# Performance work log

Measured on AMD Instinct MI355X. Metric: run time of the kernel, lower is better.

The kernel has to match this reference:

```python
import jax, jax.numpy as jnp
import numpy as np

B, T, C, H = 512, 256, 384, 64  # batch, seq (block_size), n_embd, head_size
SCALE = C ** 0.5  # NOTE: source multiplies by C**0.5 (faithful to original)


def setup_inputs() -> dict:
    key = jax.random.key(0)
    kx, kq, kk, kv = jax.random.split(key, 4)
    lim = 1.0 / np.sqrt(C)
    return {
        "x": jax.random.normal(kx, (B, T, C), dtype=jnp.float32),
        "Wq": jax.random.uniform(kq, (C, H), jnp.float32, -lim, lim),
        "Wk": jax.random.uniform(kk, (C, H), jnp.float32, -lim, lim),
        "Wv": jax.random.uniform(kv, (C, H), jnp.float32, -lim, lim),
    }


def reference(x, Wq, Wk, Wv):
    q = jnp.einsum("btc,ch->bth", x, Wq)
    k = jnp.einsum("btc,ch->bth", x, Wk)
    v = jnp.einsum("btc,ch->bth", x, Wv)
    wei = jnp.einsum("bth,bsh->bts", q, k) * SCALE  # [B,T,T]
    causal = jnp.tril(jnp.ones((T, T), dtype=bool))
    wei = jnp.where(causal, wei, -jnp.inf)
    wei = jax.nn.softmax(wei, axis=-1)
    # dropout is identity in eval mode
    out = jnp.einsum("bts,bsh->bth", wei, v)
    return out
```

## Files before the change

### kernel.cpp

```cpp
#include <hip/hip_runtime.h>
#include <math.h>

#define B_ 512
#define T_ 256
#define C_ 384
#define H_ 64

typedef __attribute__((ext_vector_type(8))) short bf16x8;
typedef __attribute__((ext_vector_type(4))) float f32x4;

#define MFMA16(a, b, c) __builtin_amdgcn_mfma_f32_16x16x32_bf16((a), (b), (c), 0, 0, 0)

#define SM_KHI   0u
#define SM_KLO   36864u
#define SM_VT    73728u
#define SM_WQH   73728u
#define SM_WQL   78848u
#define SM_WKH   83968u
#define SM_WKL   89088u
#define SM_WVH   94208u
#define SM_WVL   99328u
#define SM_XREG  107520u
#define SM_XH    107520u
#define SM_XL    128000u
#define SM_QS(s) (SM_XREG + (unsigned)(s)*9216u)
#define SM_PS(w) (SM_XREG + (unsigned)(w)*2304u)
#define SM_BYTES 148480u

static __device__ __forceinline__ unsigned short bhi(float x) {
    return (unsigned short)(__float_as_uint(x) >> 16);
}
static __device__ __forceinline__ unsigned short blo(float x) {
    float h = __uint_as_float((__float_as_uint(x) >> 16) << 16);
    return (unsigned short)(__float_as_uint(x - h) >> 16);
}
static __device__ __forceinline__ unsigned short brne(float x) {
    unsigned u = __float_as_uint(x);
    return (unsigned short)((u + 0x7FFFu + ((u >> 16) & 1u)) >> 16);
}
static __device__ __forceinline__ unsigned pk_hi(float a, float b) {
    return (unsigned)bhi(a) | ((unsigned)bhi(b) << 16);
}
static __device__ __forceinline__ unsigned pk_lo(float a, float b) {
    return (unsigned)blo(a) | ((unsigned)blo(b) << 16);
}

__global__ __launch_bounds__(512, 2)
void head_mfma(const float* __restrict__ x,
               const float* __restrict__ Wq,
               const float* __restrict__ Wk,
               const float* __restrict__ Wv,
               float* __restrict__ out)
{
    __shared__ __align__(16) unsigned char sm[SM_BYTES];

    const int tid  = threadIdx.x;
    const int b    = blockIdx.x;
    const int w    = tid >> 6;
    const int lane = tid & 63;
    const int l15  = lane & 15;
    const int quad = lane >> 4;
    const int rA   = w * 16;
    const int rB   = 240 - w * 16;

    f32x4 qac[2][4], kac[2][4], vac[2][4];
    #pragma unroll
    for (int mt = 0; mt < 2; ++mt)
        #pragma unroll
        for (int nt = 0; nt < 4; ++nt) {
            f32x4 z = {0.f, 0.f, 0.f, 0.f};
            qac[mt][nt] = z; kac[mt][nt] = z; vac[mt][nt] = z;
        }

    const int xrowi = tid >> 1;
    const int xhalf = tid & 1;
    const float* xrow = x + ((size_t)b * T_ + xrowi) * C_ + xhalf * 16;
    const int hW = tid >> 3;
    const int cg = tid & 7;

    float4 xb[4];
    float  wbq[4], wbk[4], wbv[4];
    {
        const float4* xp = (const float4*)(xrow);
        #pragma unroll
        for (int j = 0; j < 4; ++j) xb[j] = xp[j];
        const float* q0 = Wq + (size_t)(cg * 4) * H_ + hW;
        const float* k0 = Wk + (size_t)(cg * 4) * H_ + hW;
        const float* v0 = Wv + (size_t)(cg * 4) * H_ + hW;
        #pragma unroll
        for (int j = 0; j < 4; ++j) { wbq[j] = q0[j*H_]; wbk[j] = k0[j*H_]; wbv[j] = v0[j*H_]; }
    }

    #pragma unroll 1
    for (int cc = 0; cc < 12; ++cc) {
        #pragma unroll
        for (int j = 0; j < 4; ++j) {
            uint2 hh, ll;
            hh.x = pk_hi(xb[j].x, xb[j].y); hh.y = pk_hi(xb[j].z, xb[j].w);
            ll.x = pk_lo(xb[j].x, xb[j].y); ll.y = pk_lo(xb[j].z, xb[j].w);
            *(uint2*)&sm[SM_XH + (unsigned)(xrowi*80 + xhalf*32 + j*8)] = hh;
            *(uint2*)&sm[SM_XL + (unsigned)(xrowi*80 + xhalf*32 + j*8)] = ll;
        }
        {
            const unsigned wo = (unsigned)(hW*80 + cg*8);
            uint2 t;
            t.x = pk_hi(wbq[0],wbq[1]); t.y = pk_hi(wbq[2],wbq[3]); *(uint2*)&sm[SM_WQH + wo] = t;
            t.x = pk_lo(wbq[0],wbq[1]); t.y = pk_lo(wbq[2],wbq[3]); *(uint2*)&sm[SM_WQL + wo] = t;
            t.x = pk_hi(wbk[0],wbk[1]); t.y = pk_hi(wbk[2],wbk[3]); *(uint2*)&sm[SM_WKH + wo] = t;
            t.x = pk_lo(wbk[0],wbk[1]); t.y = pk_lo(wbk[2],wbk[3]); *(uint2*)&sm[SM_WKL + wo] = t;
            t.x = pk_hi(wbv[0],wbv[1]); t.y = pk_hi(wbv[2],wbv[3]); *(uint2*)&sm[SM_WVH + wo] = t;
            t.x = pk_lo(wbv[0],wbv[1]); t.y = pk_lo(wbv[2],wbv[3]); *(uint2*)&sm[SM_WVL + wo] = t;
        }
        __syncthreads();

        if (cc < 11) {
            const float4* xp = (const float4*)(xrow + (cc + 1) * 32);
            #pragma unroll
            for (int j = 0; j < 4; ++j) xb[j] = xp[j];
            const size_t c0 = (size_t)((cc + 1) * 32 + cg * 4) * H_ + hW;
            #pragma unroll
            for (int j = 0; j < 4; ++j) {
                wbq[j] = Wq[c0 + (size_t)j*H_];
                wbk[j] = Wk[c0 + (size_t)j*H_];
                wbv[j] = Wv[c0 + (size_t)j*H_];
            }
        }

        bf16x8 ah[2], al[2];
        {
            const unsigned roA = (unsigned)((rA + l15)*80 + quad*16);
            const unsigned roB = (unsigned)((rB + l15)*80 + quad*16);
            ah[0] = *(const bf16x8*)&sm[SM_XH + roA];
            al[0] = *(const bf16x8*)&sm[SM_XL + roA];
            ah[1] = *(const bf16x8*)&sm[SM_XH + roB];
            al[1] = *(const bf16x8*)&sm[SM_XL + roB];
        }
#define PROJ_MAT(WTH, WTL, ACC)                                               \
        {                                                                     \
            bf16x8 bh[4], bl[4];                                              \
            _Pragma("unroll")                                                 \
            for (int nt = 0; nt < 4; ++nt) {                                  \
                const unsigned bo = (unsigned)((nt*16 + l15)*80 + quad*16);   \
                bh[nt] = *(const bf16x8*)&sm[(WTH) + bo];                     \
                bl[nt] = *(const bf16x8*)&sm[(WTL) + bo];                     \
            }                                                                 \
            _Pragma("unroll")                                                 \
            for (int mt = 0; mt < 2; ++mt)                                    \
                _Pragma("unroll")                                             \
                for (int nt = 0; nt < 4; ++nt) {                              \
                    f32x4 a = ACC[mt][nt];                                    \
                    a = MFMA16(al[mt], bh[nt], a);                            \
                    a = MFMA16(ah[mt], bl[nt], a);                            \
                    a = MFMA16(ah[mt], bh[nt], a);                            \
                    ACC[mt][nt] = a;                                          \
                }                                                             \
        }
        PROJ_MAT(SM_WQH, SM_WQL, qac)
        PROJ_MAT(SM_WKH, SM_WKL, kac)
        PROJ_MAT(SM_WVH, SM_WVL, vac)
        __syncthreads();
    }

    constexpr float SCALE = 19.595917942265423f;
    #pragma unroll
    for (int mt = 0; mt < 2; ++mt) {
        const int r0m = mt ? rB : rA;
        #pragma unroll
        for (int nt = 0; nt < 4; ++nt) {
            const f32x4 kv = kac[mt][nt];
            const f32x4 vv = vac[mt][nt];
            #pragma unroll
            for (int r = 0; r < 4; ++r) {
                const int row = r0m + quad*4 + r;
                const int h   = nt*16 + l15;
                *(unsigned short*)&sm[SM_KHI + (unsigned)(row*144 + h*2)] = bhi(kv[r]);
                *(unsigned short*)&sm[SM_KLO + (unsigned)(row*144 + h*2)] = blo(kv[r]);
                *(unsigned short*)&sm[SM_VT  + (unsigned)(h*528 + row*2)] = brne(vv[r]);
            }
        }
    }

    bf16x8 qAh[2][2], qAl[2][2];
    const int slot = w & 3;
#define Q_XPOSE()                                                             \
    {                                                                         \
        const unsigned qb = SM_QS(slot);                                      \
        _Pragma("unroll")                                                     \
        for (int mt = 0; mt < 2; ++mt)                                        \
            _Pragma("unroll")                                                 \
            for (int nt = 0; nt < 4; ++nt) {                                  \
                const f32x4 qv = qac[mt][nt];                                 \
                _Pragma("unroll")                                             \
                for (int r = 0; r < 4; ++r) {                                 \
                    const float qs = qv[r] * SCALE;                           \
                    const int rl = mt*16 + quad*4 + r;                        \
                    const int h  = nt*16 + l15;                               \
                    *(unsigned short*)&sm[qb +         (unsigned)(rl*144 + h*2)] = bhi(qs); \
                    *(unsigned short*)&sm[qb + 4608u + (unsigned)(rl*144 + h*2)] = blo(qs); \
                }                                                             \
            }                                                                 \
        _Pragma("unroll")                                                     \
        for (int mt = 0; mt < 2; ++mt)                                        \
            _Pragma("unroll")                                                 \
            for (int ks = 0; ks < 2; ++ks) {                                  \
                const unsigned qo = (unsigned)((mt*16 + l15)*144 + ks*64 + quad*16); \
                qAh[mt][ks] = *(const bf16x8*)&sm[qb + qo];                   \
                qAl[mt][ks] = *(const bf16x8*)&sm[qb + 4608u + qo];           \
            }                                                                 \
    }
    if (w < 4) Q_XPOSE();
    __syncthreads();
    if (w >= 4) Q_XPOSE();
    __syncthreads();

    f32x4 oac[2][4];
    float m_[2][4], l_[2][4];
    #pragma unroll
    for (int mt = 0; mt < 2; ++mt) {
        #pragma unroll
        for (int nt = 0; nt < 4; ++nt) { f32x4 z = {0.f,0.f,0.f,0.f}; oac[mt][nt] = z; }
        #pragma unroll
        for (int r = 0; r < 4; ++r) { m_[mt][r] = -1e30f; l_[mt][r] = 0.f; }
    }
    const unsigned pb = SM_PS(w);

    #pragma unroll
    for (int tile = 0; tile < 2; ++tile) {
        const int r0    = tile ? rB : rA;
        const int kbmax = tile ? ((15 - w) >> 2) : (w >> 2);
        #pragma unroll 1
        for (int kb = 0; kb <= kbmax; ++kb) {
            bf16x8 kbh[4][2], kbl[4][2];
            #pragma unroll
            for (int nt = 0; nt < 4; ++nt)
                #pragma unroll
                for (int ks = 0; ks < 2; ++ks) {
                    const unsigned ko = (unsigned)((kb*64 + nt*16 + l15)*144 + ks*64 + quad*16);
                    kbh[nt][ks] = *(const bf16x8*)&sm[SM_KHI + ko];
                    kbl[nt][ks] = *(const bf16x8*)&sm[SM_KLO + ko];
                }
            f32x4 sac[4];
            #pragma unroll
            for (int nt = 0; nt < 4; ++nt) {
                f32x4 a = {0.f,0.f,0.f,0.f};
                #pragma unroll
                for (int ks = 0; ks < 2; ++ks) {
                    a = MFMA16(qAl[tile][ks], kbh[nt][ks], a);
                    a = MFMA16(qAh[tile][ks], kbl[nt][ks], a);
                    a = MFMA16(qAh[tile][ks], kbh[nt][ks], a);
                }
                sac[nt] = a;
            }
            if (kb == kbmax) {
                #pragma unroll
                for (int nt = 0; nt < 4; ++nt)
                    #pragma unroll
                    for (int r = 0; r < 4; ++r) {
                        const int rg = r0 + quad*4 + r;
                        const int kl = kb*64 + nt*16 + l15;
                        if (kl > rg) sac[nt][r] = -1e30f;
                    }
            }
            #pragma unroll
            for (int r = 0; r < 4; ++r) {
                float v = fmaxf(fmaxf(sac[0][r], sac[1][r]), fmaxf(sac[2][r], sac[3][r]));
                v = fmaxf(v, __shfl_xor(v, 1)); v = fmaxf(v, __shfl_xor(v, 2));
                v = fmaxf(v, __shfl_xor(v, 4)); v = fmaxf(v, __shfl_xor(v, 8));
                const float mnew  = fmaxf(m_[tile][r], v);
                const float alpha = __expf(m_[tile][r] - mnew);
                m_[tile][r] = mnew;
                float rs = 0.f;
                #pragma unroll
                for (int nt = 0; nt < 4; ++nt) {
                    const float p = __expf(sac[nt][r] - mnew);
                    sac[nt][r] = p;
                    rs += p;
                }
                rs += __shfl_xor(rs, 1); rs += __shfl_xor(rs, 2);
                rs += __shfl_xor(rs, 4); rs += __shfl_xor(rs, 8);
                l_[tile][r] = l_[tile][r] * alpha + rs;
                #pragma unroll
                for (int nt = 0; nt < 4; ++nt) oac[tile][nt][r] *= alpha;
                const int rl = quad*4 + r;
                #pragma unroll
                for (int nt = 0; nt < 4; ++nt)
                    *(unsigned short*)&sm[pb + (unsigned)(rl*144 + (nt*16 + l15)*2)] =
                        brne(sac[nt][r]);
            }
            bf16x8 pA[2], vB[4][2];
            #pragma unroll
            for (int ks = 0; ks < 2; ++ks)
                pA[ks] = *(const bf16x8*)&sm[pb + (unsigned)(l15*144 + ks*64 + quad*16)];
            #pragma unroll
            for (int nt = 0; nt < 4; ++nt)
                #pragma unroll
                for (int ks = 0; ks < 2; ++ks)
                    vB[nt][ks] = *(const bf16x8*)&sm[SM_VT + (unsigned)((nt*16 + l15)*528 + kb*128 + ks*64 + quad*16)];
            #pragma unroll
            for (int nt = 0; nt < 4; ++nt) {
                f32x4 a = oac[tile][nt];
                a = MFMA16(pA[0], vB[nt][0], a);
                a = MFMA16(pA[1], vB[nt][1], a);
                oac[tile][nt] = a;
            }
        }
    }

    float* ob = out + (size_t)b * (T_ * H_);
    #pragma unroll
    for (int mt = 0; mt < 2; ++mt) {
        const int r0m = mt ? rB : rA;
        float inv[4];
        #pragma unroll
        for (int r = 0; r < 4; ++r) inv[r] = 1.0f / l_[mt][r];
        #pragma unroll
        for (int nt = 0; nt < 4; ++nt)
            #pragma unroll
            for (int r = 0; r < 4; ++r) {
                const int row = r0m + quad*4 + r;
                const int h   = nt*16 + l15;
                ob[row*64 + h] = oac[mt][nt][r] * inv[r];
            }
    }
}

extern "C" void kernel_launch(void* const* d_in, const int* in_sizes, int n_in,
                              void* d_out, int out_size, void* d_ws, size_t ws_size,
                              hipStream_t stream)
{
    const float* x  = (const float*)d_in[0];
    const float* Wq = (const float*)d_in[1];
    const float* Wk = (const float*)d_in[2];
    const float* Wv = (const float*)d_in[3];
    head_mfma<<<dim3(B_), dim3(512), 0, stream>>>(x, Wq, Wk, Wv, (float*)d_out);
}
```

Measured before the change: 330.0 us.

## Double block to 1024 threads with one 16-row tile per wave

The block grows from 512 to 1024 threads, so each of 16 waves now owns a single 16-row query tile. Previously each of 8 waves handled a balanced pair of tiles (rows w*16 and 240-w*16). Projection staging, Q transpose slots and attention loops are re-indexed for the finer split, which halves accumulators per wave and doubles the waves available to hide latency. In exchange, causal work is now uneven across waves (1 to 4 key blocks each), and the 1024-thread launch bound caps registers per wave.

```diff
diff --git a/kernel.cpp b/kernel.cpp
--- a/kernel.cpp
+++ b/kernel.cpp
@@ -23,7 +23,7 @@
 #define SM_XREG  107520u
 #define SM_XH    107520u
 #define SM_XL    128000u
-#define SM_QS(s) (SM_XREG + (unsigned)(s)*9216u)
+#define SM_QS(s) (SM_XREG + (unsigned)(s)*4608u)
 #define SM_PS(w) (SM_XREG + (unsigned)(w)*2304u)
 #define SM_BYTES 148480u
 
@@ -45,7 +45,7 @@
     return (unsigned)blo(a) | ((unsigned)blo(b) << 16);
 }
 
-__global__ __launch_bounds__(512, 2)
+__global__ __launch_bounds__(1024, 4)
 void head_mfma(const float* __restrict__ x,
                const float* __restrict__ Wq,
                const float* __restrict__ Wk,
@@ -61,79 +61,70 @@
     const int l15  = lane & 15;
     const int quad = lane >> 4;
     const int rA   = w * 16;
-    const int rB   = 240 - w * 16;
-
-    f32x4 qac[2][4], kac[2][4], vac[2][4];
-    #pragma unroll
-    for (int mt = 0; mt < 2; ++mt)
-        #pragma unroll
-        for (int nt = 0; nt < 4; ++nt) {
-            f32x4 z = {0.f, 0.f, 0.f, 0.f};
-            qac[mt][nt] = z; kac[mt][nt] = z; vac[mt][nt] = z;
-        }
-
-    const int xrowi = tid >> 1;
-    const int xhalf = tid & 1;
-    const float* xrow = x + ((size_t)b * T_ + xrowi) * C_ + xhalf * 16;
-    const int hW = tid >> 3;
-    const int cg = tid & 7;
-
-    float4 xb[4];
-    float  wbq[4], wbk[4], wbv[4];
+
+    f32x4 qac[4], kac[4], vac[4];
+    #pragma unroll
+    for (int nt = 0; nt < 4; ++nt) {
+        f32x4 z = {0.f, 0.f, 0.f, 0.f};
+        qac[nt] = z; kac[nt] = z; vac[nt] = z;
+    }
+
+    const int xrowi = tid >> 2;
+    const int xq    = tid & 3;
+    const float* xrow = x + ((size_t)b * T_ + xrowi) * C_ + xq * 8;
+    const int hW = tid >> 4;
+    const int cg = tid & 15;
+
+    float4 xb[2];
+    float  wbq[2], wbk[2], wbv[2];
     {
         const float4* xp = (const float4*)(xrow);
-        #pragma unroll
-        for (int j = 0; j < 4; ++j) xb[j] = xp[j];
-        const float* q0 = Wq + (size_t)(cg * 4) * H_ + hW;
-        const float* k0 = Wk + (size_t)(cg * 4) * H_ + hW;
-        const float* v0 = Wv + (size_t)(cg * 4) * H_ + hW;
-        #pragma unroll
-        for (int j = 0; j < 4; ++j) { wbq[j] = q0[j*H_]; wbk[j] = k0[j*H_]; wbv[j] = v0[j*H_]; }
+        xb[0] = xp[0]; xb[1] = xp[1];
+        const float* q0 = Wq + (size_t)(cg * 2) * H_ + hW;
+        const float* k0 = Wk + (size_t)(cg * 2) * H_ + hW;
+        const float* v0 = Wv + (size_t)(cg * 2) * H_ + hW;
+        #pragma unroll
+        for (int j = 0; j < 2; ++j) { wbq[j] = q0[j*H_]; wbk[j] = k0[j*H_]; wbv[j] = v0[j*H_]; }
     }
 
     #pragma unroll 1
     for (int cc = 0; cc < 12; ++cc) {
         #pragma unroll
-        for (int j = 0; j < 4; ++j) {
+        for (int j = 0; j < 2; ++j) {
             uint2 hh, ll;
             hh.x = pk_hi(xb[j].x, xb[j].y); hh.y = pk_hi(xb[j].z, xb[j].w);
             ll.x = pk_lo(xb[j].x, xb[j].y); ll.y = pk_lo(xb[j].z, xb[j].w);
-            *(uint2*)&sm[SM_XH + (unsigned)(xrowi*80 + xhalf*32 + j*8)] = hh;
-            *(uint2*)&sm[SM_XL + (unsigned)(xrowi*80 + xhalf*32 + j*8)] = ll;
+            *(uint2*)&sm[SM_XH + (unsigned)(xrowi*80 + xq*16 + j*8)] = hh;
+            *(uint2*)&sm[SM_XL + (unsigned)(xrowi*80 + xq*16 + j*8)] = ll;
         }
         {
-            const unsigned wo = (unsigned)(hW*80 + cg*8);
-            uint2 t;
-            t.x = pk_hi(wbq[0],wbq[1]); t.y = pk_hi(wbq[2],wbq[3]); *(uint2*)&sm[SM_WQH + wo] = t;
-            t.x = pk_lo(wbq[0],wbq[1]); t.y = pk_lo(wbq[2],wbq[3]); *(uint2*)&sm[SM_WQL + wo] = t;
-            t.x = pk_hi(wbk[0],wbk[1]); t.y = pk_hi(wbk[2],wbk[3]); *(uint2*)&sm[SM_WKH + wo] = t;
-            t.x = pk_lo(wbk[0],wbk[1]); t.y = pk_lo(wbk[2],wbk[3]); *(uint2*)&sm[SM_WKL + wo] = t;
-            t.x = pk_hi(wbv[0],wbv[1]); t.y = pk_hi(wbv[2],wbv[3]); *(uint2*)&sm[SM_WVH + wo] = t;
-            t.x = pk_lo(wbv[0],wbv[1]); t.y = pk_lo(wbv[2],wbv[3]); *(uint2*)&sm[SM_WVL + wo] = t;
+            const unsigned wo = (unsigned)(hW*80 + cg*4);
+            *(unsigned*)&sm[SM_WQH + wo] = pk_hi(wbq[0], wbq[1]);
+            *(unsigned*)&sm[SM_WQL + wo] = pk_lo(wbq[0], wbq[1]);
+            *(unsigned*)&sm[SM_WKH + wo] = pk_hi(wbk[0], wbk[1]);
+            *(unsigned*)&sm[SM_WKL + wo] = pk_lo(wbk[0], wbk[1]);
+            *(unsigned*)&sm[SM_WVH + wo] = pk_hi(wbv[0], wbv[1]);
+            *(unsigned*)&sm[SM_WVL + wo] = pk_lo(wbv[0], wbv[1]);
         }
         __syncthreads();
 
         if (cc < 11) {
             const float4* xp = (const float4*)(xrow + (cc + 1) * 32);
-            #pragma unroll
-            for (int j = 0; j < 4; ++j) xb[j] = xp[j];
-            const size_t c0 = (size_t)((cc + 1) * 32 + cg * 4) * H_ + hW;
-            #pragma unroll
-            for (int j = 0; j < 4; ++j) {
+            xb[0] = xp[0]; xb[1] = xp[1];
+            const size_t c0 = (size_t)((cc + 1) * 32 + cg * 2) * H_ + hW;
+            #pragma unroll
+            for (int j = 0; j < 2; ++j) {
                 wbq[j] = Wq[c0 + (size_t)j*H_];
                 wbk[j] = Wk[c0 + (size_t)j*H_];
                 wbv[j] = Wv[c0 + (size_t)j*H_];
             }
         }
 
-        bf16x8 ah[2], al[2];
+        bf16x8 ah, al;
         {
-            const unsigned roA = (unsigned)((rA + l15)*80 + quad*16);
-            const unsigned roB = (unsigned)((rB + l15)*80 + quad*16);
-            ah[0] = *(const bf16x8*)&sm[SM_XH + roA];
-            al[0] = *(const bf16x8*)&sm[SM_XL + roA];
-            ah[1] = *(const bf16x8*)&sm[SM_XH + roB];
-            al[1] = *(const bf16x8*)&sm[SM_XL + roB];
+            const unsigned ro = (unsigned)((rA + l15)*80 + quad*16);
+            ah = *(const bf16x8*)&sm[SM_XH + ro];
+            al = *(const bf16x8*)&sm[SM_XL + ro];
         }
 #define PROJ_MAT(WTH, WTL, ACC)                                               \
         {                                                                     \
@@ -145,15 +136,13 @@
                 bl[nt] = *(const bf16x8*)&sm[(WTL) + bo];                     \
             }                                                                 \
             _Pragma("unroll")                                                 \
-            for (int mt = 0; mt < 2; ++mt)                                    \
-                _Pragma("unroll")                                             \
-                for (int nt = 0; nt < 4; ++nt) {                              \
-                    f32x4 a = ACC[mt][nt];                                    \
-                    a = MFMA16(al[mt], bh[nt], a);                            \
-                    a = MFMA16(ah[mt], bl[nt], a);                            \
-                    a = MFMA16(ah[mt], bh[nt], a);                            \
-                    ACC[mt][nt] = a;                                          \
-                }                                                             \
+            for (int nt = 0; nt < 4; ++nt) {                                  \
+                f32x4 a = ACC[nt];                                            \
+                a = MFMA16(al, bh[nt], a);                                    \
+                a = MFMA16(ah, bl[nt], a);                                    \
+                a = MFMA16(ah, bh[nt], a);                                    \
+                ACC[nt] = a;                                                  \
+            }                                                                 \
         }
         PROJ_MAT(SM_WQH, SM_WQL, qac)
         PROJ_MAT(SM_WKH, SM_WKL, kac)
@@ -163,165 +152,146 @@
 
     constexpr float SCALE = 19.595917942265423f;
     #pragma unroll
-    for (int mt = 0; mt < 2; ++mt) {
-        const int r0m = mt ? rB : rA;
-        #pragma unroll
-        for (int nt = 0; nt < 4; ++nt) {
-            const f32x4 kv = kac[mt][nt];
-            const f32x4 vv = vac[mt][nt];
-            #pragma unroll
-            for (int r = 0; r < 4; ++r) {
-                const int row = r0m + quad*4 + r;
-                const int h   = nt*16 + l15;
-                *(unsigned short*)&sm[SM_KHI + (unsigned)(row*144 + h*2)] = bhi(kv[r]);
-                *(unsigned short*)&sm[SM_KLO + (unsigned)(row*144 + h*2)] = blo(kv[r]);
-                *(unsigned short*)&sm[SM_VT  + (unsigned)(h*528 + row*2)] = brne(vv[r]);
-            }
-        }
-    }
-
-    bf16x8 qAh[2][2], qAl[2][2];
-    const int slot = w & 3;
+    for (int nt = 0; nt < 4; ++nt) {
+        const f32x4 kv = kac[nt];
+        const f32x4 vv = vac[nt];
+        #pragma unroll
+        for (int r = 0; r < 4; ++r) {
+            const int row = rA + quad*4 + r;
+            const int h   = nt*16 + l15;
+            *(unsigned short*)&sm[SM_KHI + (unsigned)(row*144 + h*2)] = bhi(kv[r]);
+            *(unsigned short*)&sm[SM_KLO + (unsigned)(row*144 + h*2)] = blo(kv[r]);
+            *(unsigned short*)&sm[SM_VT  + (unsigned)(h*528 + row*2)] = brne(vv[r]);
+        }
+    }
+
+    bf16x8 qAh[2], qAl[2];
+    const int slot = w & 7;
 #define Q_XPOSE()                                                             \
     {                                                                         \
         const unsigned qb = SM_QS(slot);                                      \
         _Pragma("unroll")                                                     \
-        for (int mt = 0; mt < 2; ++mt)                                        \
+        for (int nt = 0; nt < 4; ++nt) {                                      \
+            const f32x4 qv = qac[nt];                                         \
             _Pragma("unroll")                                                 \
-            for (int nt = 0; nt < 4; ++nt) {                                  \
-                const f32x4 qv = qac[mt][nt];                                 \
-                _Pragma("unroll")                                             \
-                for (int r = 0; r < 4; ++r) {                                 \
-                    const float qs = qv[r] * SCALE;                           \
-                    const int rl = mt*16 + quad*4 + r;                        \
-                    const int h  = nt*16 + l15;                               \
-                    *(unsigned short*)&sm[qb +         (unsigned)(rl*144 + h*2)] = bhi(qs); \
-                    *(unsigned short*)&sm[qb + 4608u + (unsigned)(rl*144 + h*2)] = blo(qs); \
-                }                                                             \
+            for (int r = 0; r < 4; ++r) {                                     \
+                const float qs = qv[r] * SCALE;                               \
+                const int rl = quad*4 + r;                                    \
+                const int h  = nt*16 + l15;                                   \
+                *(unsigned short*)&sm[qb +         (unsigned)(rl*144 + h*2)] = bhi(qs); \
+                *(unsigned short*)&sm[qb + 2304u + (unsigned)(rl*144 + h*2)] = blo(qs); \
             }                                                                 \
+        }                                                                     \
         _Pragma("unroll")                                                     \
-        for (int mt = 0; mt < 2; ++mt)                                        \
-            _Pragma("unroll")                                                 \
-            for (int ks = 0; ks < 2; ++ks) {                                  \
-                const unsigned qo = (unsigned)((mt*16 + l15)*144 + ks*64 + quad*16); \
-                qAh[mt][ks] = *(const bf16x8*)&sm[qb + qo];                   \
-                qAl[mt][ks] = *(const bf16x8*)&sm[qb + 4608u + qo];           \
-            }                                                                 \
-    }
-    if (w < 4) Q_XPOSE();
+        for (int ks = 0; ks < 2; ++ks) {                                      \
+            const unsigned qo = (unsigned)(l15*144 + ks*64 + quad*16);        \
+            qAh[ks] = *(const bf16x8*)&sm[qb + qo];                           \
+            qAl[ks] = *(const bf16x8*)&sm[qb + 2304u + qo];                   \
+        }                                                                     \
+    }
+    if (w < 8) Q_XPOSE();
     __syncthreads();
-    if (w >= 4) Q_XPOSE();
+    if (w >= 8) Q_XPOSE();
     __syncthreads();
 
-    f32x4 oac[2][4];
-    float m_[2][4], l_[2][4];
-    #pragma unroll
-    for (int mt = 0; mt < 2; ++mt) {
-        #pragma unroll
-        for (int nt = 0; nt < 4; ++nt) { f32x4 z = {0.f,0.f,0.f,0.f}; oac[mt][nt] = z; }
-        #pragma unroll
-        for (int r = 0; r < 4; ++r) { m_[mt][r] = -1e30f; l_[mt][r] = 0.f; }
-    }
+    f32x4 oac[4];
+    float m_[4], l_[4];
+    #pragma unroll
+    for (int nt = 0; nt < 4; ++nt) { f32x4 z = {0.f,0.f,0.f,0.f}; oac[nt] = z; }
+    #pragma unroll
+    for (int r = 0; r < 4; ++r) { m_[r] = -1e30f; l_[r] = 0.f; }
     const unsigned pb = SM_PS(w);
-
-    #pragma unroll
-    for (int tile = 0; tile < 2; ++tile) {
-        const int r0    = tile ? rB : rA;
-        const int kbmax = tile ? ((15 - w) >> 2) : (w >> 2);
-        #pragma unroll 1
-        for (int kb = 0; kb <= kbmax; ++kb) {
-            bf16x8 kbh[4][2], kbl[4][2];
+    const int kbmax = w >> 2;
+
+    #pragma unroll 1
+    for (int kb = 0; kb <= kbmax; ++kb) {
+        bf16x8 kbh[4][2], kbl[4][2];
+        #pragma unroll
+        for (int nt = 0; nt < 4; ++nt)
+            #pragma unroll
+            for (int ks = 0; ks < 2; ++ks) {
+                const unsigned ko = (unsigned)((kb*64 + nt*16 + l15)*144 + ks*64 + quad*16);
+                kbh[nt][ks] = *(const bf16x8*)&sm[SM_KHI + ko];
+                kbl[nt][ks] = *(const bf16x8*)&sm[SM_KLO + ko];
+            }
+        f32x4 sac[4];
+        #pragma unroll
+        for (int nt = 0; nt < 4; ++nt) {
+            f32x4 a = {0.f,0.f,0.f,0.f};
+            #pragma unroll
+            for (int ks = 0; ks < 2; ++ks) {
+                a = MFMA16(qAl[ks], kbh[nt][ks], a);
+                a = MFMA16(qAh[ks], kbl[nt][ks], a);
+                a = MFMA16(qAh[ks], kbh[nt][ks], a);
+            }
+            sac[nt] = a;
+        }
+        if (kb == kbmax) {
             #pragma unroll
             for (int nt = 0; nt < 4; ++nt)
                 #pragma unroll
-                for (int ks = 0; ks < 2; ++ks) {
-                    const unsigned ko = (unsigned)((kb*64 + nt*16 + l15)*144 + ks*64 + quad*16);
-                    kbh[nt][ks] = *(const bf16x8*)&sm[SM_KHI + ko];
-                    kbl[nt][ks] = *(const bf16x8*)&sm[SM_KLO + ko];
+                for (int r = 0; r < 4; ++r) {
+                    const int rg = rA + quad*4 + r;
+                    const int kl = kb*64 + nt*16 + l15;
+                    if (kl > rg) sac[nt][r] = -1e30f;
                 }
-            f32x4 sac[4];
+        }
+        #pragma unroll
+        for (int r = 0; r < 4; ++r) {
+            float v = fmaxf(fmaxf(sac[0][r], sac[1][r]), fmaxf(sac[2][r], sac[3][r]));
+            v = fmaxf(v, __shfl_xor(v, 1)); v = fmaxf(v, __shfl_xor(v, 2));
+            v = fmaxf(v, __shfl_xor(v, 4)); v = fmaxf(v, __shfl_xor(v, 8));
+            const float mnew  = fmaxf(m_[r], v);
+            const float alpha = __expf(m_[r] - mnew);
+            m_[r] = mnew;
+            float rs = 0.f;
             #pragma unroll
             for (int nt = 0; nt < 4; ++nt) {
-                f32x4 a = {0.f,0.f,0.f,0.f};
-                #pragma unroll
-                for (int ks = 0; ks < 2; ++ks) {
-                    a = MFMA16(qAl[tile][ks], kbh[nt][ks], a);
-                    a = MFMA16(qAh[tile][ks], kbl[nt][ks], a);
-                    a = MFMA16(qAh[tile][ks], kbh[nt][ks], a);
-                }
-                sac[nt] = a;
+                const float p = __expf(sac[nt][r] - mnew);
+                sac[nt][r] = p;
+                rs += p;
             }
-            if (kb == kbmax) {
-                #pragma unroll
-                for (int nt = 0; nt < 4; ++nt)
-                    #pragma unroll
-                    for (int r = 0; r < 4; ++r) {
-                        const int rg = r0 + quad*4 + r;
-                        const int kl = kb*64 + nt*16 + l15;
-                        if (kl > rg) sac[nt][r] = -1e30f;
-                    }
-            }
-            #pragma unroll
-            for (int r = 0; r < 4; ++r) {
-                float v = fmaxf(fmaxf(sac[0][r], sac[1][r]), fmaxf(sac[2][r], sac[3][r]));
-                v = fmaxf(v, __shfl_xor(v, 1)); v = fmaxf(v, __shfl_xor(v, 2));
-                v = fmaxf(v, __shfl_xor(v, 4)); v = fmaxf(v, __shfl_xor(v, 8));
-                const float mnew  = fmaxf(m_[tile][r], v);
-                const float alpha = __expf(m_[tile][r] - mnew);
-                m_[tile][r] = mnew;
-                float rs = 0.f;
-                #pragma unroll
-                for (int nt = 0; nt < 4; ++nt) {
-                    const float p = __expf(sac[nt][r] - mnew);
-                    sac[nt][r] = p;
-                    rs += p;
-                }
-                rs += __shfl_xor(rs, 1); rs += __shfl_xor(rs, 2);
-                rs += __shfl_xor(rs, 4); rs += __shfl_xor(rs, 8);
-                l_[tile][r] = l_[tile][r] * alpha + rs;
-                #pragma unroll
-                for (int nt = 0; nt < 4; ++nt) oac[tile][nt][r] *= alpha;
-                const int rl = quad*4 + r;
-                #pragma unroll
-                for (int nt = 0; nt < 4; ++nt)
-                    *(unsigned short*)&sm[pb + (unsigned)(rl*144 + (nt*16 + l15)*2)] =
-                        brne(sac[nt][r]);
-            }
-            bf16x8 pA[2], vB[4][2];
+            rs += __shfl_xor(rs, 1); rs += __shfl_xor(rs, 2);
+            rs += __shfl_xor(rs, 4); rs += __shfl_xor(rs, 8);
+            l_[r] = l_[r] * alpha + rs;
+            #pragma unroll
+            for (int nt = 0; nt < 4; ++nt) oac[nt][r] *= alpha;
+            const int rl = quad*4 + r;
+            #pragma unroll
+            for (int nt = 0; nt < 4; ++nt)
+                *(unsigned short*)&sm[pb + (unsigned)(rl*144 + (nt*16 + l15)*2)] =
+                    brne(sac[nt][r]);
+        }
+        bf16x8 pA[2], vB[4][2];
+        #pragma unroll
+        for (int ks = 0; ks < 2; ++ks)
+            pA[ks] = *(const bf16x8*)&sm[pb + (unsigned)(l15*144 + ks*64 + quad*16)];
+        #pragma unroll
+        for (int nt = 0; nt < 4; ++nt)
             #pragma unroll
             for (int ks = 0; ks < 2; ++ks)
-                pA[ks] = *(const bf16x8*)&sm[pb + (unsigned)(l15*144 + ks*64 + quad*16)];
-            #pragma unroll
-            for (int nt = 0; nt < 4; ++nt)
-                #pragma unroll
-                for (int ks = 0; ks < 2; ++ks)
-                    vB[nt][ks] = *(const bf16x8*)&sm[SM_VT + (unsigned)((nt*16 + l15)*528 + kb*128 + ks*64 + quad*16)];
-            #pragma unroll
-            for (int nt = 0; nt < 4; ++nt) {
-                f32x4 a = oac[tile][nt];
-                a = MFMA16(pA[0], vB[nt][0], a);
-                a = MFMA16(pA[1], vB[nt][1], a);
-                oac[tile][nt] = a;
-            }
+                vB[nt][ks] = *(const bf16x8*)&sm[SM_VT + (unsigned)((nt*16 + l15)*528 + kb*128 + ks*64 + quad*16)];
+        #pragma unroll
+        for (int nt = 0; nt < 4; ++nt) {
+            f32x4 a = oac[nt];
+            a = MFMA16(pA[0], vB[nt][0], a);
+            a = MFMA16(pA[1], vB[nt][1], a);
+            oac[nt] = a;
         }
     }
 
     float* ob = out + (size_t)b * (T_ * H_);
-    #pragma unroll
-    for (int mt = 0; mt < 2; ++mt) {
-        const int r0m = mt ? rB : rA;
-        float inv[4];
-        #pragma unroll
-        for (int r = 0; r < 4; ++r) inv[r] = 1.0f / l_[mt][r];
-        #pragma unroll
-        for (int nt = 0; nt < 4; ++nt)
-            #pragma unroll
-            for (int r = 0; r < 4; ++r) {
-                const int row = r0m + quad*4 + r;
-                const int h   = nt*16 + l15;
-                ob[row*64 + h] = oac[mt][nt][r] * inv[r];
-            }
-    }
+    float inv[4];
+    #pragma unroll
+    for (int r = 0; r < 4; ++r) inv[r] = 1.0f / l_[r];
+    #pragma unroll
+    for (int nt = 0; nt < 4; ++nt)
+        #pragma unroll
+        for (int r = 0; r < 4; ++r) {
+            const int row = rA + quad*4 + r;
+            const int h   = nt*16 + l15;
+            ob[row*64 + h] = oac[nt][r] * inv[r];
+        }
 }
 
 extern "C" void kernel_launch(void* const* d_in, const int* in_sizes, int n_in,
@@ -332,5 +302,5 @@
     const float* Wq = (const float*)d_in[1];
     const float* Wk = (const float*)d_in[2];
     const float* Wv = (const float*)d_in[3];
-    head_mfma<<<dim3(B_), dim3(512), 0, stream>>>(x, Wq, Wk, Wv, (float*)d_out);
-}
+    head_mfma<<<dim3(B_), dim3(1024), 0, stream>>>(x, Wq, Wk, Wv, (float*)d_out);
+}
```

Result: slower. 369.9 us (+12.1%).

## Prepack weights to bf16 hi/lo in workspace and double-buffer projection staging

Applied to the files above, without the earlier changes.

Adds a small pre-kernel that converts Wq/Wk/Wv into split bf16 hi/lo tiles laid out as the MFMA loop expects, so each block copies weight chunks with wide 16-byte loads instead of strided scalar loads plus per-block conversion. The projection loop now double-buffers the x and weight shared-memory tiles, filling the next chunk while computing the current one, which removes one barrier per iteration. This costs an extra kernel launch and depends on the workspace buffer, and the larger shared-memory staging area could constrain occupancy.

```diff
diff --git a/kernel.cpp b/kernel.cpp
--- a/kernel.cpp
+++ b/kernel.cpp
@@ -11,21 +11,17 @@
 
 #define MFMA16(a, b, c) __builtin_amdgcn_mfma_f32_16x16x32_bf16((a), (b), (c), 0, 0, 0)
 
+#define BUFSZ    73728u
+#define XH_OFF   0u
+#define XL_OFF   20480u
+#define W_OFF    40960u
 #define SM_KHI   0u
 #define SM_KLO   36864u
 #define SM_VT    73728u
-#define SM_WQH   73728u
-#define SM_WQL   78848u
-#define SM_WKH   83968u
-#define SM_WKL   89088u
-#define SM_WVH   94208u
-#define SM_WVL   99328u
-#define SM_XREG  107520u
-#define SM_XH    107520u
-#define SM_XL    128000u
-#define SM_QS(s) (SM_XREG + (unsigned)(s)*9216u)
-#define SM_PS(w) (SM_XREG + (unsigned)(w)*2304u)
-#define SM_BYTES 148480u
+#define SM_QS(s) (107520u + (unsigned)(s)*9216u)
+#define SM_PS(w) (107520u + (unsigned)(w)*2304u)
+#define SM_BYTES 147456u
+#define WCHUNK   32768u
 
 static __device__ __forceinline__ unsigned short bhi(float x) {
     return (unsigned short)(__float_as_uint(x) >> 16);
@@ -45,11 +41,28 @@
     return (unsigned)blo(a) | ((unsigned)blo(b) << 16);
 }
 
+__global__ __launch_bounds__(256)
+void wprep(const float* __restrict__ Wq, const float* __restrict__ Wk,
+           const float* __restrict__ Wv, unsigned char* __restrict__ ws)
+{
+    const int cc = blockIdx.x / 3, m = blockIdx.x % 3;
+    const float* W = (m == 0) ? Wq : (m == 1) ? Wk : Wv;
+    const int tid = threadIdx.x;
+    const int c   = tid >> 3;
+    const int h0  = (tid & 7) * 8;
+    const float* src = W + (size_t)(cc * 32 + c) * H_ + h0;
+    unsigned char* dst = ws + (size_t)cc * WCHUNK + (size_t)m * 10240u;
+    #pragma unroll
+    for (int j = 0; j < 8; ++j) {
+        const float v = src[j];
+        *(unsigned short*)(dst +         (unsigned)((h0 + j) * 80 + c * 2)) = bhi(v);
+        *(unsigned short*)(dst + 5120u + (unsigned)((h0 + j) * 80 + c * 2)) = blo(v);
+    }
+}
+
 __global__ __launch_bounds__(512, 2)
 void head_mfma(const float* __restrict__ x,
-               const float* __restrict__ Wq,
-               const float* __restrict__ Wk,
-               const float* __restrict__ Wv,
+               const unsigned char* __restrict__ wpack,
                float* __restrict__ out)
 {
     __shared__ __align__(16) unsigned char sm[SM_BYTES];
@@ -75,54 +88,54 @@
     const int xrowi = tid >> 1;
     const int xhalf = tid & 1;
     const float* xrow = x + ((size_t)b * T_ + xrowi) * C_ + xhalf * 16;
-    const int hW = tid >> 3;
-    const int cg = tid & 7;
 
     float4 xb[4];
-    float  wbq[4], wbk[4], wbv[4];
+
+#define X_PACK(BUF)                                                           \
+    {                                                                         \
+        _Pragma("unroll")                                                     \
+        for (int j = 0; j < 4; ++j) {                                         \
+            uint2 hh, ll;                                                     \
+            hh.x = pk_hi(xb[j].x, xb[j].y); hh.y = pk_hi(xb[j].z, xb[j].w);   \
+            ll.x = pk_lo(xb[j].x, xb[j].y); ll.y = pk_lo(xb[j].z, xb[j].w);   \
+            *(uint2*)&sm[(BUF) + XH_OFF + (unsigned)(xrowi*80 + xhalf*32 + j*8)] = hh; \
+            *(uint2*)&sm[(BUF) + XL_OFF + (unsigned)(xrowi*80 + xhalf*32 + j*8)] = ll; \
+        }                                                                     \
+    }
+
     {
-        const float4* xp = (const float4*)(xrow);
+        const float4* xp = (const float4*)xrow;
         #pragma unroll
         for (int j = 0; j < 4; ++j) xb[j] = xp[j];
-        const float* q0 = Wq + (size_t)(cg * 4) * H_ + hW;
-        const float* k0 = Wk + (size_t)(cg * 4) * H_ + hW;
-        const float* v0 = Wv + (size_t)(cg * 4) * H_ + hW;
-        #pragma unroll
-        for (int j = 0; j < 4; ++j) { wbq[j] = q0[j*H_]; wbk[j] = k0[j*H_]; wbv[j] = v0[j*H_]; }
-    }
+        const uint4* wsrc = (const uint4*)(wpack);
+        uint4 wt0 = wsrc[tid], wt1 = wsrc[512 + tid], wt2 = wsrc[1024 + tid], wt3 = wsrc[1536 + tid];
+        X_PACK(0u)
+        *(uint4*)&sm[W_OFF + (unsigned)tid * 16u]           = wt0;
+        *(uint4*)&sm[W_OFF + (unsigned)(512  + tid) * 16u]  = wt1;
+        *(uint4*)&sm[W_OFF + (unsigned)(1024 + tid) * 16u]  = wt2;
+        *(uint4*)&sm[W_OFF + (unsigned)(1536 + tid) * 16u]  = wt3;
+        const float4* xp1 = (const float4*)(xrow + 32);
+        #pragma unroll
+        for (int j = 0; j < 4; ++j) xb[j] = xp1[j];
+    }
+    __syncthreads();
 
     #pragma unroll 1
     for (int cc = 0; cc < 12; ++cc) {
-        #pragma unroll
-        for (int j = 0; j < 4; ++j) {
-            uint2 hh, ll;
-            hh.x = pk_hi(xb[j].x, xb[j].y); hh.y = pk_hi(xb[j].z, xb[j].w);
-            ll.x = pk_lo(xb[j].x, xb[j].y); ll.y = pk_lo(xb[j].z, xb[j].w);
-            *(uint2*)&sm[SM_XH + (unsigned)(xrowi*80 + xhalf*32 + j*8)] = hh;
-            *(uint2*)&sm[SM_XL + (unsigned)(xrowi*80 + xhalf*32 + j*8)] = ll;
-        }
-        {
-            const unsigned wo = (unsigned)(hW*80 + cg*8);
-            uint2 t;
-            t.x = pk_hi(wbq[0],wbq[1]); t.y = pk_hi(wbq[2],wbq[3]); *(uint2*)&sm[SM_WQH + wo] = t;
-            t.x = pk_lo(wbq[0],wbq[1]); t.y = pk_lo(wbq[2],wbq[3]); *(uint2*)&sm[SM_WQL + wo] = t;
-            t.x = pk_hi(wbk[0],wbk[1]); t.y = pk_hi(wbk[2],wbk[3]); *(uint2*)&sm[SM_WKH + wo] = t;
-            t.x = pk_lo(wbk[0],wbk[1]); t.y = pk_lo(wbk[2],wbk[3]); *(uint2*)&sm[SM_WKL + wo] = t;
-            t.x = pk_hi(wbv[0],wbv[1]); t.y = pk_hi(wbv[2],wbv[3]); *(uint2*)&sm[SM_WVH + wo] = t;
-            t.x = pk_lo(wbv[0],wbv[1]); t.y = pk_lo(wbv[2],wbv[3]); *(uint2*)&sm[SM_WVL + wo] = t;
-        }
-        __syncthreads();
-
+        const unsigned bc = (unsigned)(cc & 1) * BUFSZ;
         if (cc < 11) {
-            const float4* xp = (const float4*)(xrow + (cc + 1) * 32);
-            #pragma unroll
-            for (int j = 0; j < 4; ++j) xb[j] = xp[j];
-            const size_t c0 = (size_t)((cc + 1) * 32 + cg * 4) * H_ + hW;
-            #pragma unroll
-            for (int j = 0; j < 4; ++j) {
-                wbq[j] = Wq[c0 + (size_t)j*H_];
-                wbk[j] = Wk[c0 + (size_t)j*H_];
-                wbv[j] = Wv[c0 + (size_t)j*H_];
+            const unsigned bn = BUFSZ - bc;
+            const uint4* wsrc = (const uint4*)(wpack + (size_t)(cc + 1) * WCHUNK);
+            uint4 wt0 = wsrc[tid], wt1 = wsrc[512 + tid], wt2 = wsrc[1024 + tid], wt3 = wsrc[1536 + tid];
+            X_PACK(bn)
+            *(uint4*)&sm[bn + W_OFF + (unsigned)tid * 16u]           = wt0;
+            *(uint4*)&sm[bn + W_OFF + (unsigned)(512  + tid) * 16u]  = wt1;
+            *(uint4*)&sm[bn + W_OFF + (unsigned)(1024 + tid) * 16u]  = wt2;
+            *(uint4*)&sm[bn + W_OFF + (unsigned)(1536 + tid) * 16u]  = wt3;
+            if (cc < 10) {
+                const float4* xp = (const float4*)(xrow + (cc + 2) * 32);
+                #pragma unroll
+                for (int j = 0; j < 4; ++j) xb[j] = xp[j];
             }
         }
 
@@ -130,10 +143,10 @@
         {
             const unsigned roA = (unsigned)((rA + l15)*80 + quad*16);
             const unsigned roB = (unsigned)((rB + l15)*80 + quad*16);
-            ah[0] = *(const bf16x8*)&sm[SM_XH + roA];
-            al[0] = *(const bf16x8*)&sm[SM_XL + roA];
-            ah[1] = *(const bf16x8*)&sm[SM_XH + roB];
-            al[1] = *(const bf16x8*)&sm[SM_XL + roB];
+            ah[0] = *(const bf16x8*)&sm[bc + XH_OFF + roA];
+            al[0] = *(const bf16x8*)&sm[bc + XL_OFF + roA];
+            ah[1] = *(const bf16x8*)&sm[bc + XH_OFF + roB];
+            al[1] = *(const bf16x8*)&sm[bc + XL_OFF + roB];
         }
 #define PROJ_MAT(WTH, WTL, ACC)                                               \
         {                                                                     \
@@ -155,9 +168,9 @@
                     ACC[mt][nt] = a;                                          \
                 }                                                             \
         }
-        PROJ_MAT(SM_WQH, SM_WQL, qac)
-        PROJ_MAT(SM_WKH, SM_WKL, kac)
-        PROJ_MAT(SM_WVH, SM_WVL, vac)
+        PROJ_MAT(bc + W_OFF +     0u, bc + W_OFF +  5120u, qac)
+        PROJ_MAT(bc + W_OFF + 10240u, bc + W_OFF + 15360u, kac)
+        PROJ_MAT(bc + W_OFF + 20480u, bc + W_OFF + 25600u, vac)
         __syncthreads();
     }
 
@@ -332,5 +345,7 @@
     const float* Wq = (const float*)d_in[1];
     const float* Wk = (const float*)d_in[2];
     const float* Wv = (const float*)d_in[3];
-    head_mfma<<<dim3(B_), dim3(512), 0, stream>>>(x, Wq, Wk, Wv, (float*)d_out);
-}
+    wprep<<<dim3(36), dim3(256), 0, stream>>>(Wq, Wk, Wv, (unsigned char*)d_ws);
+    head_mfma<<<dim3(B_), dim3(512), 0, stream>>>(x, (const unsigned char*)d_ws,
+                                                  (float*)d_out);
+}
```

Result: faster. 321.7 us (-2.5%).
